# Kernel optimization log

Hardware: AMD Instinct MI355X
Metric: run time of the kernel (lower is better)

The kernel has to match this reference:

```python
import jax, jax.numpy as jnp
import numpy as np

C32 = 768      # channels at stride 32 (convnextv2)
E = 4          # num_experts


def setup_inputs() -> dict:
    key = jax.random.key(0)
    ks = jax.random.split(key, 12)
    s = 0.02
    inp = {
        "s4":  jax.random.normal(ks[0], (8, 96, 256, 256), jnp.float32),
        "s8":  jax.random.normal(ks[1], (8, 192, 128, 128), jnp.float32),
        "s16": jax.random.normal(ks[2], (8, 384, 64, 64), jnp.float32),
        "s32": jax.random.normal(ks[3], (8, C32, 32, 32), jnp.float32),
        # 2-layer gate: C -> C -> E
        "gate_w1": jax.random.normal(ks[4], (C32, C32), jnp.float32) * s,
        "gate_b1": jnp.zeros((C32,), jnp.float32),
        "gate_w2": jax.random.normal(ks[5], (C32, E), jnp.float32) * s,
        "gate_b2": jnp.zeros((E,), jnp.float32),
        # E stacked ProtoExpert MLPs: C -> C -> C
        "exp_w1": jax.random.normal(ks[6], (E, C32, C32), jnp.float32) * s,
        "exp_b1": jnp.zeros((E, C32), jnp.float32),
        "exp_w2": jax.random.normal(ks[7], (E, C32, C32), jnp.float32) * s,
        "exp_b2": jnp.zeros((E, C32), jnp.float32),
    }
    return inp


def _vision_moe(x_bchw, gate_w1, gate_b1, gate_w2, gate_b2, exp_w1, exp_b1, exp_w2, exp_b2):
    B, C, H, W = x_bchw.shape
    x = x_bchw.transpose(0, 2, 3, 1).reshape(-1, C)            # [N, C] tokens
    # 2-layer gate -> softmax -> top-1 routing
    logits = jax.nn.gelu(x @ gate_w1 + gate_b1) @ gate_w2 + gate_b2  # [N, E]
    probs = jax.nn.softmax(logits, axis=-1)
    top_idx = jnp.argmax(probs, axis=-1)                        # [N]
    gate_val = jnp.take_along_axis(probs, top_idx[:, None], axis=-1)  # [N, 1]
    # dense all-expert compute, then select routed expert (jit-friendly)
    h = jax.nn.gelu(jnp.einsum('nc,ecd->ned', x, exp_w1) + exp_b1)    # [N, E, C]
    y_all = jnp.einsum('ned,edf->nef', h, exp_w2) + exp_b2            # [N, E, C]
    onehot = jax.nn.one_hot(top_idx, probs.shape[-1], dtype=x.dtype)  # [N, E]
    y = jnp.einsum('nef,ne->nf', y_all, onehot) * gate_val            # [N, C]
    return y.reshape(B, H, W, C).transpose(0, 3, 1, 2)


def reference(s4, s8, s16, s32, gate_w1, gate_b1, gate_w2, gate_b2, exp_w1, exp_b1, exp_w2, exp_b2):
    out32 = _vision_moe(s32, gate_w1, gate_b1, gate_w2, gate_b2,
                        exp_w1, exp_b1, exp_w2, exp_b2) + s32
    return (s4, s8, s16, out32)
```

## Files before the change

kernel.cpp:

```cpp
#include <hip/hip_runtime.h>
#include <cstddef>

#define CCH 768
#define CHUNK 262144u

#define OFF_YT    0u
#define OFF_HH    12582912u
#define OFF_W2T   25165824u
#define OFF_AUX   29884416u
#define OFF_PART  30146560u
#define OFF_XH    31719424u
#define OFF_GWH   44302336u
#define OFF_GWL   45481984u
#define OFF_XL    46661632u
#define OFF_W1T   59244544u
#define TAILBYTES 12582912u

typedef __attribute__((ext_vector_type(8))) short short8v;
typedef __attribute__((ext_vector_type(4))) float f32x4;

__device__ __forceinline__ void gl16(const void* g, void* l) {
    __builtin_amdgcn_global_load_lds(
        (const __attribute__((address_space(1))) void*)g,
        (__attribute__((address_space(3))) void*)l, 16, 0, 0);
}

__device__ __forceinline__ void copy_chunk(int g, const char* s4b, const char* s8b,
                                           const char* s16b, char* bb) {
    const char* src = (g < 768) ? s4b + (size_t)g * CHUNK
                    : (g < 1152) ? s8b + (size_t)(g - 768) * CHUNK
                                 : s16b + (size_t)(g - 1152) * CHUNK;
    const uint4* s = (const uint4*)src;
    uint4* d = (uint4*)(bb + (size_t)g * CHUNK);
    int t = threadIdx.x;
#pragma unroll 8
    for (int it = 0; it < 64; ++it) d[it * 256 + t] = s[it * 256 + t];
}

__device__ __forceinline__ float gelu_tanh(float x) {
    float u = 0.7978845608028654f * (x + 0.044715f * x * x * x);
    float e = __expf(2.0f * u);
    float t = 1.0f - 2.0f / (e + 1.0f);
    return 0.5f * x * (1.0f + t);
}

__device__ __forceinline__ short f2b(float f) {
    unsigned u = __float_as_uint(f);
    unsigned r = (u + 0x7FFFu + ((u >> 16) & 1u)) >> 16;
    return (short)r;
}

__device__ __forceinline__ float b2f(short s) {
    return __uint_as_float(((unsigned)(unsigned short)s) << 16);
}

__global__ __launch_bounds__(256) void k_prep(const float* __restrict__ s32,
                                              const float* __restrict__ gw1,
                                              short* __restrict__ Xh,
                                              short* __restrict__ Xl,
                                              short* __restrict__ GWh,
                                              short* __restrict__ GWl,
                                              int* __restrict__ az) {
    int z = blockIdx.z;
    int tx = threadIdx.x, ty = threadIdx.y;
    if (z == 0 && blockIdx.x == 0 && blockIdx.y == 0 && ty == 0 && tx < 16)
        az[tx] = 0;
    __shared__ float tile[32][33];
    if (z < 8) {
        int c0 = blockIdx.y * 32, hw0 = blockIdx.x * 32;
        const float* s = s32 + (size_t)z * CCH * 1024;
#pragma unroll
        for (int i = 0; i < 4; ++i)
            tile[ty + 8 * i][tx] = s[(size_t)(c0 + ty + 8 * i) * 1024 + hw0 + tx];
        __syncthreads();
#pragma unroll
        for (int i = 0; i < 4; ++i) {
            int r = ty + 8 * i;
            int n = z * 1024 + hw0 + r;
            float v = tile[tx][r];
            short h = f2b(v);
            Xh[(size_t)n * CCH + c0 + tx] = h;
            Xl[(size_t)n * CCH + c0 + tx] = f2b(v - b2f(h));
        }
    } else {
        if (blockIdx.x >= 24) return;
        int ci0 = blockIdx.x * 32, co0 = blockIdx.y * 32;
#pragma unroll
        for (int i = 0; i < 4; ++i)
            tile[ty + 8 * i][tx] = gw1[(size_t)(ci0 + ty + 8 * i) * CCH + co0 + tx];
        __syncthreads();
#pragma unroll
        for (int i = 0; i < 4; ++i) {
            int co = co0 + ty + 8 * i;
            float v = tile[tx][ty + 8 * i];
            short h = f2b(v);
            GWh[(size_t)co * CCH + ci0 + tx] = h;
            GWl[(size_t)co * CCH + ci0 + tx] = f2b(v - b2f(h));
        }
    }
}

template <int MODE>
__global__ __launch_bounds__(256) void k_mfma(const short* __restrict__ Ahp,
                                              const short* __restrict__ Alp,
                                              const short* __restrict__ Bhp,
                                              const short* __restrict__ Blp,
                                              const float* __restrict__ bias,
                                              const float* __restrict__ gw2,
                                              const int* __restrict__ perm,
                                              const int* __restrict__ counts,
                                              const float* __restrict__ gval,
                                              short* __restrict__ Yt,
                                              short* __restrict__ Hout,
                                              float* __restrict__ partial,
                                              const float* __restrict__ ew1,
                                              const float* __restrict__ ew2,
                                              short* __restrict__ W1T,
                                              short* __restrict__ W2T,
                                              const char* __restrict__ s4b,
                                              const char* __restrict__ s8b,
                                              const char* __restrict__ s16b,
                                              char* __restrict__ bb,
                                              int ngemm, int ncopy) {
    __shared__ __align__(16) short lds[32768];
    int bid = blockIdx.x;
    int t = threadIdx.x;
    if (bid >= ngemm) {
        int i = bid - ngemm;
        if (i < ncopy) {
            int g;
            if (MODE == 0) g = 244 + i;
            else if (MODE == 1) g = (i < 57) ? 169 + i : 744 + (i - 57);
            else g = (i < 48) ? 121 + i : (i < 66) ? 226 + (i - 48) : 1024 + (i - 66);
            copy_chunk(g, s4b, s8b, s16b, bb);
        } else if (MODE == 0) {
            int j = i - ncopy;
            int mat = j / 576, q = j % 576;
            int ci0 = (q % 24) * 32, co0 = (q / 24) * 32;
            const float* src = (mat < 4 ? ew1 : ew2) + (size_t)(mat & 3) * CCH * CCH;
            short* dst = (mat < 4 ? W1T : W2T) + (size_t)(mat & 3) * CCH * CCH;
            float* tile = (float*)lds;
            int tx = t & 31, ty = t >> 5;
#pragma unroll
            for (int i4 = 0; i4 < 4; ++i4)
                tile[(ty + 8 * i4) * 33 + tx] =
                    src[(size_t)(ci0 + ty + 8 * i4) * CCH + co0 + tx];
            __syncthreads();
#pragma unroll
            for (int i4 = 0; i4 < 4; ++i4) {
                int co = co0 + ty + 8 * i4;
                dst[(size_t)co * CCH + ci0 + tx] = f2b(tile[tx * 33 + ty + 8 * i4]);
            }
        }
        return;
    }

    int cbk = bid % 6;
    int mt = bid / 6;
    int c0 = cbk * 128;
    int e = 0, ts = mt, cnt = 1 << 30, ofs = 0, mrow0 = 0;
    if (MODE == 0) {
        mrow0 = mt * 128;
    } else {
        e = mt >> 6;
        ts = mt & 63;
        int n0 = counts[0], n1 = counts[1], n2 = counts[2], n3 = counts[3];
        cnt = (e == 0) ? n0 : (e == 1) ? n1 : (e == 2) ? n2 : n3;
        if (ts * 128 >= cnt) return;
        ofs = (e > 0 ? n0 : 0) + (e > 1 ? n1 : 0) + (e > 2 ? n2 : 0);
    }

    int lane = t & 63, w = t >> 6;
    int wr = w >> 1, wc = w & 1;
    int lrow = lane & 15, lk8 = lane >> 4;

    const short* aS[4];
    const short* bS[4];
    const short* alS[2];
    const short* blS[2];
    int dA[4];

    if (MODE == 0) {
#pragma unroll
        for (int i = 0; i < 2; ++i) {
            int c = 2 * w + i;
            int row = c * 16 + lrow;
            int koff = lk8 * 8;
            aS[i]  = Ahp + (size_t)(mrow0 + row) * CCH + koff;
            alS[i] = Alp + (size_t)(mrow0 + row) * CCH + koff;
            bS[i]  = Bhp + (size_t)(c0 + row) * CCH + koff;
            blS[i] = Blp + (size_t)(c0 + row) * CCH + koff;
            dA[i] = c * 512;
        }
    } else {
        size_t eoff = (size_t)e * CCH * CCH;
#pragma unroll
        for (int i = 0; i < 4; ++i) {
            int c = 4 * w + i;
            int g = c >> 1, ph = c & 1;
            int row = g * 16 + lrow;
            int koff = ph * 32 + lk8 * 8;
            int pl = ts * 128 + row;
            int pc = pl < cnt ? pl : cnt - 1;
            int arow = (MODE == 1) ? perm[ofs + pc] : (ofs + pc);
            aS[i] = Ahp + (size_t)arow * CCH + koff;
            bS[i] = Bhp + eoff + (size_t)(c0 + row) * CCH + koff;
            dA[i] = c * 512;
        }
    }

    f32x4 acc[4][4] = {};

    if (MODE == 0) {
        auto stage = [&](int b, int k0) {
            short* L = lds + b * 16384;
#pragma unroll
            for (int i = 0; i < 2; ++i) {
                gl16(aS[i] + k0, L + dA[i]);
                gl16(bS[i] + k0, L + 4096 + dA[i]);
                gl16(alS[i] + k0, L + 8192 + dA[i]);
                gl16(blS[i] + k0, L + 12288 + dA[i]);
            }
        };
        stage(0, 0);
        __syncthreads();
        for (int tt = 0; tt < 24; ++tt) {
            int cur = tt & 1;
            if (tt < 23) stage(cur ^ 1, (tt + 1) * 32);
            const short* L = lds + cur * 16384;
            short8v af[4], bf[4], xf[4];
#pragma unroll
            for (int m = 0; m < 4; ++m)
                af[m] = *(const short8v*)(L + ((wr * 4 + m) * 64 + lane) * 8);
#pragma unroll
            for (int n = 0; n < 4; ++n)
                bf[n] = *(const short8v*)(L + 4096 + ((wc * 4 + n) * 64 + lane) * 8);
#pragma unroll
            for (int m = 0; m < 4; ++m)
#pragma unroll
                for (int n = 0; n < 4; ++n)
                    acc[m][n] = __builtin_amdgcn_mfma_f32_16x16x32_bf16(af[m], bf[n], acc[m][n], 0, 0, 0);
#pragma unroll
            for (int n = 0; n < 4; ++n)
                xf[n] = *(const short8v*)(L + 12288 + ((wc * 4 + n) * 64 + lane) * 8);
#pragma unroll
            for (int m = 0; m < 4; ++m)
#pragma unroll
                for (int n = 0; n < 4; ++n)
                    acc[m][n] = __builtin_amdgcn_mfma_f32_16x16x32_bf16(af[m], xf[n], acc[m][n], 0, 0, 0);
#pragma unroll
            for (int m = 0; m < 4; ++m)
                xf[m] = *(const short8v*)(L + 8192 + ((wr * 4 + m) * 64 + lane) * 8);
#pragma unroll
            for (int m = 0; m < 4; ++m)
#pragma unroll
                for (int n = 0; n < 4; ++n)
                    acc[m][n] = __builtin_amdgcn_mfma_f32_16x16x32_bf16(xf[m], bf[n], acc[m][n], 0, 0, 0);
            __syncthreads();
        }
    } else {
        auto stage = [&](int b, int k0) {
            short* L = lds + b * 16384;
#pragma unroll
            for (int i = 0; i < 4; ++i) {
                gl16(aS[i] + k0, L + dA[i]);
                gl16(bS[i] + k0, L + 8192 + dA[i]);
            }
        };
        stage(0, 0);
        __syncthreads();
        for (int tt = 0; tt < 12; ++tt) {
            int cur = tt & 1;
            if (tt < 11) stage(cur ^ 1, (tt + 1) * 64);
            const short* L = lds + cur * 16384;
#pragma unroll
            for (int kk = 0; kk < 2; ++kk) {
                short8v af[4], bf[4];
#pragma unroll
                for (int m = 0; m < 4; ++m)
                    af[m] = *(const short8v*)(L + (((wr * 4 + m) * 2 + kk) * 64 + lane) * 8);
#pragma unroll
                for (int n = 0; n < 4; ++n)
                    bf[n] = *(const short8v*)(L + 8192 + (((wc * 4 + n) * 2 + kk) * 64 + lane) * 8);
#pragma unroll
                for (int m = 0; m < 4; ++m)
#pragma unroll
                    for (int n = 0; n < 4; ++n)
                        acc[m][n] = __builtin_amdgcn_mfma_f32_16x16x32_bf16(af[m], bf[n], acc[m][n], 0, 0, 0);
            }
            __syncthreads();
        }
    }

    int cl = lane & 15, rh = (lane >> 4) * 4;
    if (MODE == 0) {
        int cb2 = cbk * 2 + wc;
        float bv[4];
        float4 w2v[4];
#pragma unroll
        for (int n_ = 0; n_ < 4; ++n_) {
            int col = c0 + wc * 64 + n_ * 16 + cl;
            bv[n_] = bias[col];
            w2v[n_] = *(const float4*)(gw2 + col * 4);
        }
#pragma unroll
        for (int m = 0; m < 4; ++m) {
#pragma unroll
            for (int ri = 0; ri < 4; ++ri) {
                float s0 = 0.f, s1 = 0.f, s2 = 0.f, s3 = 0.f;
#pragma unroll
                for (int n_ = 0; n_ < 4; ++n_) {
                    float g = gelu_tanh(acc[m][n_][ri] + bv[n_]);
                    s0 = fmaf(g, w2v[n_].x, s0);
                    s1 = fmaf(g, w2v[n_].y, s1);
                    s2 = fmaf(g, w2v[n_].z, s2);
                    s3 = fmaf(g, w2v[n_].w, s3);
                }
#pragma unroll
                for (int off = 1; off < 16; off <<= 1) {
                    s0 += __shfl_xor(s0, off);
                    s1 += __shfl_xor(s1, off);
                    s2 += __shfl_xor(s2, off);
                    s3 += __shfl_xor(s3, off);
                }
                if (cl == 0) {
                    int row = mrow0 + wr * 64 + m * 16 + rh + ri;
                    float4 pv;
                    pv.x = s0; pv.y = s1; pv.z = s2; pv.w = s3;
                    *(float4*)(partial + (size_t)(cb2 * 8192 + row) * 4) = pv;
                }
            }
        }
    } else {
#pragma unroll
        for (int n = 0; n < 4; ++n) {
            int col = c0 + wc * 64 + n * 16 + cl;
            float bv = bias[e * CCH + col];
#pragma unroll
            for (int m = 0; m < 4; ++m) {
#pragma unroll
                for (int ri = 0; ri < 4; ++ri) {
                    int p = ts * 128 + wr * 64 + m * 16 + rh + ri;
                    if (p < cnt) {
                        float v = acc[m][n][ri] + bv;
                        if (MODE == 1) {
                            Hout[(size_t)(ofs + p) * CCH + col] = f2b(gelu_tanh(v));
                        } else {
                            int nn = perm[ofs + p];
                            Yt[(size_t)nn * CCH + col] = f2b(v * gval[nn]);
                        }
                    }
                }
            }
        }
    }
}

__global__ __launch_bounds__(256) void k_route(const float* __restrict__ partial,
                                               const float* __restrict__ b2,
                                               int* __restrict__ idx,
                                               float* __restrict__ gval,
                                               int* __restrict__ counts) {
    int n = blockIdx.x * 256 + threadIdx.x;
    float l0 = b2[0], l1 = b2[1], l2 = b2[2], l3 = b2[3];
#pragma unroll
    for (int p = 0; p < 12; ++p) {
        float4 v = *(const float4*)(partial + ((size_t)p * 8192 + n) * 4);
        l0 += v.x; l1 += v.y; l2 += v.z; l3 += v.w;
    }
    int e = 0;
    float m = l0;
    if (l1 > m) { m = l1; e = 1; }
    if (l2 > m) { m = l2; e = 2; }
    if (l3 > m) { m = l3; e = 3; }
    float s = __expf(l0 - m) + __expf(l1 - m) + __expf(l2 - m) + __expf(l3 - m);
    idx[n] = e;
    gval[n] = 1.0f / s;
    atomicAdd(counts + e, 1);
}

__global__ __launch_bounds__(256) void k_scatter(const int* __restrict__ idx,
                                                 const int* __restrict__ counts,
                                                 int* __restrict__ cursors,
                                                 int* __restrict__ perm) {
    int n = blockIdx.x * 256 + threadIdx.x;
    int e = idx[n];
    int run = 0;
#pragma unroll
    for (int ee = 0; ee < 4; ++ee) {
        int c = counts[ee];
        if (e == ee) {
            int pos = run + atomicAdd(cursors + ee, 1);
            perm[pos] = n;
        }
        run += c;
    }
}

__global__ __launch_bounds__(256) void k_untr(const short* __restrict__ Yt,
                                              const float* __restrict__ s32,
                                              float* __restrict__ out32,
                                              const char* __restrict__ s4b,
                                              const char* __restrict__ s8b,
                                              const char* __restrict__ s16b,
                                              char* __restrict__ bb,
                                              int ncopy) {
    int bid = blockIdx.x;
    if (bid >= 6144) {
        int i = bid - 6144;
        if (i < ncopy) {
            int g = (i < 73) ? 48 + i : 1274 + (i - 73);
            copy_chunk(g, s4b, s8b, s16b, bb);
        }
        return;
    }
    __shared__ float tile[32][33];
    int hw0 = (bid & 31) * 32;
    int c0 = ((bid >> 5) % 24) * 32;
    int b = bid / 768;
    int t = threadIdx.x;
    int tx = t & 31, ty = t >> 5;
#pragma unroll
    for (int i = 0; i < 4; ++i) {
        int hwl = ty + 8 * i;
        tile[hwl][tx] = b2f(Yt[(size_t)(b * 1024 + hw0 + hwl) * CCH + c0 + tx]);
    }
    __syncthreads();
    const float* sp = s32 + (size_t)b * CCH * 1024;
    float* op = out32 + (size_t)b * CCH * 1024;
#pragma unroll
    for (int i = 0; i < 4; ++i) {
        size_t a = (size_t)(c0 + ty + 8 * i) * 1024 + hw0 + tx;
        op[a] = tile[tx][ty + 8 * i] + sp[a];
    }
}

extern "C" void kernel_launch(void* const* d_in, const int* in_sizes, int n_in,
                              void* d_out, int out_size, void* d_ws, size_t ws_size,
                              hipStream_t stream) {
    const float* s4  = (const float*)d_in[0];
    const float* s8  = (const float*)d_in[1];
    const float* s16 = (const float*)d_in[2];
    const float* s32 = (const float*)d_in[3];
    const float* gw1 = (const float*)d_in[4];
    const float* gb1 = (const float*)d_in[5];
    const float* gw2 = (const float*)d_in[6];
    const float* gb2 = (const float*)d_in[7];
    const float* ew1 = (const float*)d_in[8];
    const float* eb1 = (const float*)d_in[9];
    const float* ew2 = (const float*)d_in[10];
    const float* eb2 = (const float*)d_in[11];

    char* bb = (char*)d_out;
    short* Yt      = (short*)(bb + OFF_YT);
    short* Hh      = (short*)(bb + OFF_HH);
    short* W2T     = (short*)(bb + OFF_W2T);
    int*   iaux    = (int*)(bb + OFF_AUX);
    int*   idx     = iaux;
    int*   perm    = iaux + 8192;
    int*   counts  = iaux + 16384;
    int*   cursors = iaux + 16388;
    float* gval    = (float*)(iaux + 16400);
    float* partial = (float*)(bb + OFF_PART);
    short* Xh      = (short*)(bb + OFF_XH);
    short* GWh     = (short*)(bb + OFF_GWH);
    short* GWl     = (short*)(bb + OFF_GWL);
    short* Xl      = (short*)(bb + OFF_XL);
    short* W1T     = (short*)(bb + OFF_W1T);
    float* out32   = (float*)(bb + (size_t)1344 * CHUNK);

    k_prep<<<dim3(32, 24, 9), dim3(32, 8), 0, stream>>>(s32, gw1, Xh, Xl, GWh, GWl,
                                                        iaux + 16384);
    k_mfma<0><<<384 + 500 + 4608, 256, 0, stream>>>(Xh, Xl, GWh, GWl, gb1, gw2,
                                                    perm, counts, gval, Yt, Hh,
                                                    partial, ew1, ew2, W1T, W2T,
                                                    (const char*)s4, (const char*)s8,
                                                    (const char*)s16, bb, 384, 500);
    k_route<<<32, 256, 0, stream>>>(partial, gb2, idx, gval, counts);
    k_scatter<<<32, 256, 0, stream>>>(idx, counts, cursors, perm);
    k_mfma<1><<<1536 + 337, 256, 0, stream>>>(Xh, Xl, W1T, GWl, eb1, gw2,
                                              perm, counts, gval, Yt, Hh,
                                              partial, ew1, ew2, W1T, W2T,
                                              (const char*)s4, (const char*)s8,
                                              (const char*)s16, bb, 1536, 337);
    k_mfma<2><<<1536 + 316, 256, 0, stream>>>(Hh, Xl, W2T, GWl, eb2, gw2,
                                              perm, counts, gval, Yt, Hh,
                                              partial, ew1, ew2, W1T, W2T,
                                              (const char*)s4, (const char*)s8,
                                              (const char*)s16, bb, 1536, 316);
    k_untr<<<6144 + 143, 256, 0, stream>>>(Yt, s32, out32, (const char*)s4,
                                           (const char*)s8, (const char*)s16, bb, 143);
    hipMemcpyAsync(bb, s4, (size_t)TAILBYTES, hipMemcpyDeviceToDevice, stream);
}
```

Before: 454.6 us.

## Fuse scatter into routing, store fp32 Yt, rebalance passthrough copy across kernels

Removes the separate scatter kernel. Routing now writes token indices straight into per-expert buckets of fixed stride 8192 using an atomic cursor, so the expert GEMMs index perm by expert instead of by prefix offset. The routed output Yt is stored as fp32 instead of bf16, and the untranspose kernel no longer carries copy blocks. The workspace layout and the split of passthrough chunk copies are redone: more copy blocks go into the gate GEMM launch and the final memcpy tail grows. Token order inside each bucket is nondeterministic, and Yt traffic doubles.

```diff
diff --git a/kernel.cpp b/kernel.cpp
--- a/kernel.cpp
+++ b/kernel.cpp
@@ -5,16 +5,16 @@
 #define CHUNK 262144u
 
 #define OFF_YT    0u
-#define OFF_HH    12582912u
-#define OFF_W2T   25165824u
-#define OFF_AUX   29884416u
-#define OFF_PART  30146560u
-#define OFF_XH    31719424u
-#define OFF_GWH   44302336u
-#define OFF_GWL   45481984u
-#define OFF_XL    46661632u
-#define OFF_W1T   59244544u
-#define TAILBYTES 12582912u
+#define OFF_HH    25165824u
+#define OFF_W2T   37748736u
+#define OFF_AUX   42467328u
+#define OFF_PART  42631424u
+#define TAILBYTES 44564480u
+#define OFF_XL    44564480u
+#define OFF_GWH   57147392u
+#define OFF_GWL   58327040u
+#define OFF_XH    59506688u
+#define OFF_W1T   72089600u
 
 typedef __attribute__((ext_vector_type(8))) short short8v;
 typedef __attribute__((ext_vector_type(4))) float f32x4;
@@ -63,7 +63,7 @@
                                               int* __restrict__ az) {
     int z = blockIdx.z;
     int tx = threadIdx.x, ty = threadIdx.y;
-    if (z == 0 && blockIdx.x == 0 && blockIdx.y == 0 && ty == 0 && tx < 16)
+    if (z == 0 && blockIdx.x == 0 && blockIdx.y == 0 && ty == 0 && tx < 8)
         az[tx] = 0;
     __shared__ float tile[32][33];
     if (z < 8) {
@@ -110,7 +110,7 @@
                                               const int* __restrict__ perm,
                                               const int* __restrict__ counts,
                                               const float* __restrict__ gval,
-                                              short* __restrict__ Yt,
+                                              float* __restrict__ Yt,
                                               short* __restrict__ Hout,
                                               float* __restrict__ partial,
                                               const float* __restrict__ ew1,
@@ -129,9 +129,9 @@
         int i = bid - ngemm;
         if (i < ncopy) {
             int g;
-            if (MODE == 0) g = 244 + i;
-            else if (MODE == 1) g = (i < 57) ? 169 + i : 744 + (i - 57);
-            else g = (i < 48) ? 121 + i : (i < 66) ? 226 + (i - 48) : 1024 + (i - 66);
+            if (MODE == 0) g = (i < 475) ? 293 + i : 768 + (i - 475);
+            else if (MODE == 1) g = (i < 57) ? 170 + i : 1152 + (i - 57);
+            else g = (i < 66) ? 227 + i : 1248 + (i - 66);
             copy_chunk(g, s4b, s8b, s16b, bb);
         } else if (MODE == 0) {
             int j = i - ncopy;
@@ -202,7 +202,7 @@
             int koff = ph * 32 + lk8 * 8;
             int pl = ts * 128 + row;
             int pc = pl < cnt ? pl : cnt - 1;
-            int arow = (MODE == 1) ? perm[ofs + pc] : (ofs + pc);
+            int arow = (MODE == 1) ? perm[e * 8192 + pc] : (ofs + pc);
             aS[i] = Ahp + (size_t)arow * CCH + koff;
             bS[i] = Bhp + eoff + (size_t)(c0 + row) * CCH + koff;
             dA[i] = c * 512;
@@ -346,8 +346,8 @@
                         if (MODE == 1) {
                             Hout[(size_t)(ofs + p) * CCH + col] = f2b(gelu_tanh(v));
                         } else {
-                            int nn = perm[ofs + p];
-                            Yt[(size_t)nn * CCH + col] = f2b(v * gval[nn]);
+                            int nn = perm[e * 8192 + p];
+                            Yt[(size_t)nn * CCH + col] = v * gval[nn];
                         }
                     }
                 }
@@ -358,7 +358,7 @@
 
 __global__ __launch_bounds__(256) void k_route(const float* __restrict__ partial,
                                                const float* __restrict__ b2,
-                                               int* __restrict__ idx,
+                                               int* __restrict__ perm,
                                                float* __restrict__ gval,
                                                int* __restrict__ counts) {
     int n = blockIdx.x * 256 + threadIdx.x;
@@ -374,56 +374,22 @@
     if (l2 > m) { m = l2; e = 2; }
     if (l3 > m) { m = l3; e = 3; }
     float s = __expf(l0 - m) + __expf(l1 - m) + __expf(l2 - m) + __expf(l3 - m);
-    idx[n] = e;
     gval[n] = 1.0f / s;
-    atomicAdd(counts + e, 1);
-}
-
-__global__ __launch_bounds__(256) void k_scatter(const int* __restrict__ idx,
-                                                 const int* __restrict__ counts,
-                                                 int* __restrict__ cursors,
-                                                 int* __restrict__ perm) {
-    int n = blockIdx.x * 256 + threadIdx.x;
-    int e = idx[n];
-    int run = 0;
-#pragma unroll
-    for (int ee = 0; ee < 4; ++ee) {
-        int c = counts[ee];
-        if (e == ee) {
-            int pos = run + atomicAdd(cursors + ee, 1);
-            perm[pos] = n;
-        }
-        run += c;
-    }
-}
-
-__global__ __launch_bounds__(256) void k_untr(const short* __restrict__ Yt,
+    int pos = atomicAdd(counts + e, 1);
+    perm[e * 8192 + pos] = n;
+}
+
+__global__ __launch_bounds__(256) void k_untr(const float* __restrict__ Yt,
                                               const float* __restrict__ s32,
-                                              float* __restrict__ out32,
-                                              const char* __restrict__ s4b,
-                                              const char* __restrict__ s8b,
-                                              const char* __restrict__ s16b,
-                                              char* __restrict__ bb,
-                                              int ncopy) {
-    int bid = blockIdx.x;
-    if (bid >= 6144) {
-        int i = bid - 6144;
-        if (i < ncopy) {
-            int g = (i < 73) ? 48 + i : 1274 + (i - 73);
-            copy_chunk(g, s4b, s8b, s16b, bb);
-        }
-        return;
-    }
+                                              float* __restrict__ out32) {
     __shared__ float tile[32][33];
-    int hw0 = (bid & 31) * 32;
-    int c0 = ((bid >> 5) % 24) * 32;
-    int b = bid / 768;
-    int t = threadIdx.x;
-    int tx = t & 31, ty = t >> 5;
+    int b = blockIdx.z;
+    int c0 = blockIdx.y * 32, hw0 = blockIdx.x * 32;
+    int tx = threadIdx.x, ty = threadIdx.y;
 #pragma unroll
     for (int i = 0; i < 4; ++i) {
         int hwl = ty + 8 * i;
-        tile[hwl][tx] = b2f(Yt[(size_t)(b * 1024 + hw0 + hwl) * CCH + c0 + tx]);
+        tile[hwl][tx] = Yt[(size_t)(b * 1024 + hw0 + hwl) * CCH + c0 + tx];
     }
     __syncthreads();
     const float* sp = s32 + (size_t)b * CCH * 1024;
@@ -452,43 +418,39 @@
     const float* eb2 = (const float*)d_in[11];
 
     char* bb = (char*)d_out;
-    short* Yt      = (short*)(bb + OFF_YT);
+    float* Yt      = (float*)(bb + OFF_YT);
     short* Hh      = (short*)(bb + OFF_HH);
     short* W2T     = (short*)(bb + OFF_W2T);
     int*   iaux    = (int*)(bb + OFF_AUX);
-    int*   idx     = iaux;
-    int*   perm    = iaux + 8192;
-    int*   counts  = iaux + 16384;
-    int*   cursors = iaux + 16388;
-    float* gval    = (float*)(iaux + 16400);
+    int*   perm    = iaux;
+    int*   counts  = iaux + 32768;
+    float* gval    = (float*)(iaux + 32776);
     float* partial = (float*)(bb + OFF_PART);
-    short* Xh      = (short*)(bb + OFF_XH);
+    short* Xl      = (short*)(bb + OFF_XL);
     short* GWh     = (short*)(bb + OFF_GWH);
     short* GWl     = (short*)(bb + OFF_GWL);
-    short* Xl      = (short*)(bb + OFF_XL);
+    short* Xh      = (short*)(bb + OFF_XH);
     short* W1T     = (short*)(bb + OFF_W1T);
     float* out32   = (float*)(bb + (size_t)1344 * CHUNK);
 
     k_prep<<<dim3(32, 24, 9), dim3(32, 8), 0, stream>>>(s32, gw1, Xh, Xl, GWh, GWl,
-                                                        iaux + 16384);
-    k_mfma<0><<<384 + 500 + 4608, 256, 0, stream>>>(Xh, Xl, GWh, GWl, gb1, gw2,
+                                                        counts);
+    k_mfma<0><<<384 + 859 + 4608, 256, 0, stream>>>(Xh, Xl, GWh, GWl, gb1, gw2,
                                                     perm, counts, gval, Yt, Hh,
                                                     partial, ew1, ew2, W1T, W2T,
                                                     (const char*)s4, (const char*)s8,
-                                                    (const char*)s16, bb, 384, 500);
-    k_route<<<32, 256, 0, stream>>>(partial, gb2, idx, gval, counts);
-    k_scatter<<<32, 256, 0, stream>>>(idx, counts, cursors, perm);
-    k_mfma<1><<<1536 + 337, 256, 0, stream>>>(Xh, Xl, W1T, GWl, eb1, gw2,
+                                                    (const char*)s16, bb, 384, 859);
+    k_route<<<32, 256, 0, stream>>>(partial, gb2, perm, gval, counts);
+    k_mfma<1><<<1536 + 153, 256, 0, stream>>>(Xh, Xl, W1T, GWl, eb1, gw2,
                                               perm, counts, gval, Yt, Hh,
                                               partial, ew1, ew2, W1T, W2T,
                                               (const char*)s4, (const char*)s8,
-                                              (const char*)s16, bb, 1536, 337);
-    k_mfma<2><<<1536 + 316, 256, 0, stream>>>(Hh, Xl, W2T, GWl, eb2, gw2,
+                                              (const char*)s16, bb, 1536, 153);
+    k_mfma<2><<<1536 + 162, 256, 0, stream>>>(Hh, Xl, W2T, GWl, eb2, gw2,
                                               perm, counts, gval, Yt, Hh,
                                               partial, ew1, ew2, W1T, W2T,
                                               (const char*)s4, (const char*)s8,
-                                              (const char*)s16, bb, 1536, 316);
-    k_untr<<<6144 + 143, 256, 0, stream>>>(Yt, s32, out32, (const char*)s4,
-                                           (const char*)s8, (const char*)s16, bb, 143);
+                                              (const char*)s16, bb, 1536, 162);
+    k_untr<<<dim3(32, 24, 8), dim3(32, 8), 0, stream>>>(Yt, s32, out32);
     hipMemcpyAsync(bb, s4, (size_t)TAILBYTES, hipMemcpyDeviceToDevice, stream);
 }
```

Result: faster. 365.3 us, median of 2 (-19.7%).
